# Kernel tuning notes

Hardware: AMD Instinct MI355X
Metric: run time of the kernel (lower is better)

The kernel has to match this reference:

```python
import jax, jax.numpy as jnp
import numpy as np

EMBEDDING_DIM = 64  # matches init_kwargs; temperature = sqrt(embedding_dim)


def setup_inputs() -> dict:
    key = jax.random.key(0)
    k1, k2, k3, k4 = jax.random.split(key, 4)
    B, S, D = 8, 2048, EMBEDDING_DIM
    return {
        "key": jax.random.normal(k1, (B, S, D), dtype=jnp.float32),
        "query": jax.random.normal(k2, (B, S, D), dtype=jnp.float32),
        "value": jax.random.normal(k3, (B, S, D), dtype=jnp.float32),
        "query_attention_mask": jax.random.randint(k4, (B, S), 0, 2, dtype=jnp.int32),
    }


def reference(key, query, value, query_attention_mask):
    # scores: [B, S, S]
    temperature = jnp.sqrt(jnp.asarray(EMBEDDING_DIM, dtype=query.dtype))
    scores = jnp.einsum("bqd,bkd->bqk", query, key) / temperature
    # masked_fill_ fills -inf WHERE mask is True (as in the torch source).
    # mask [B, S] -> broadcast over the query axis to [B, 1, S] -> [B, S, S].
    mask = query_attention_mask.astype(bool)[:, None, :]
    scores = jnp.where(mask, -jnp.inf, scores)
    attention_filter = jax.nn.softmax(scores, axis=-1)
    # dropout p=0.0 (deterministic reference) -> identity
    context = jnp.einsum("bqk,bkd->bqd", attention_filter, value)
    return (context, attention_filter)
```

## Files before the change

### kernel.cpp

```cpp
#include <hip/hip_runtime.h>
#include <hip/hip_bf16.h>
#include <math.h>


typedef short bf16x8 __attribute__((ext_vector_type(8)));
typedef short bf16x4 __attribute__((ext_vector_type(4)));
typedef float f32x4 __attribute__((ext_vector_type(4)));

#define BATCH 8
#define SDIM 2048
#define DDIM 64
#define KBLK 64
#define NBLK (SDIM / KBLK)
#define KSPLIT 4
#define BPW (NBLK / KSPLIT)
#define NROWS (BATCH * SDIM)
#define SCALE 0.125f
#define KSTR 66

__device__ __forceinline__ short f2bf(float f) {
    unsigned x = __float_as_uint(f);
    x = (x + 0x7fffu + ((x >> 16) & 1u)) >> 16;
    return (short)x;
}
__device__ __forceinline__ float fidx(const float4& v, int i) {
    return ((const float*)&v)[i];
}

__global__ __launch_bounds__(256, 4)
void attn_stats(const float* __restrict__ Kg, const float* __restrict__ Qg,
                const int* __restrict__ Mg, float* __restrict__ part)
{
    __shared__ short Klds[KBLK][KSTR];
    __shared__ int   Mlds[KBLK];

    const int wg = blockIdx.x;
    const int b = wg & 7;
    const int qt = (wg >> 3) & 31;
    const int sp = wg >> 8;
    const int tid = threadIdx.x;
    const int w = tid >> 6, lane = tid & 63, col = lane & 15, quad = lane >> 4;

    const float* Kb = Kg + (size_t)b * SDIM * DDIM;
    const float* Qb = Qg + (size_t)b * SDIM * DDIM;
    const int*   Mb = Mg + (size_t)b * SDIM;

    bf16x8 aq[2];
    {
        const float* qsrc = Qb + (size_t)(qt * 64 + w * 16 + col) * DDIM + quad * 8;
        #pragma unroll
        for (int c = 0; c < 2; ++c) {
            float4 f0 = *(const float4*)(qsrc + c * 32);
            float4 f1 = *(const float4*)(qsrc + c * 32 + 4);
            bf16x8 a;
            a[0]=f2bf(f0.x); a[1]=f2bf(f0.y); a[2]=f2bf(f0.z); a[3]=f2bf(f0.w);
            a[4]=f2bf(f1.x); a[5]=f2bf(f1.y); a[6]=f2bf(f1.z); a[7]=f2bf(f1.w);
            aq[c] = a;
        }
    }

    const int sk_key = tid >> 2;
    const int sk_d0  = (tid & 3) * 16;
    const int kb0 = sp * BPW * KBLK;

    float lsum[4];
    #pragma unroll
    for (int r = 0; r < 4; ++r) lsum[r] = 0.0f;

    float4 kreg[4];
    int mreg = 0;
    {
        const float* src = Kb + (size_t)(kb0 + sk_key) * DDIM + sk_d0;
        #pragma unroll
        for (int i = 0; i < 4; ++i) kreg[i] = *(const float4*)(src + i * 4);
        if (tid < KBLK) mreg = Mb[kb0 + tid];
    }

    for (int kb = 0; kb < BPW; ++kb) {
        __syncthreads();
        {
            bf16x8 p0, p1;
            p0[0]=f2bf(kreg[0].x); p0[1]=f2bf(kreg[0].y); p0[2]=f2bf(kreg[0].z); p0[3]=f2bf(kreg[0].w);
            p0[4]=f2bf(kreg[1].x); p0[5]=f2bf(kreg[1].y); p0[6]=f2bf(kreg[1].z); p0[7]=f2bf(kreg[1].w);
            p1[0]=f2bf(kreg[2].x); p1[1]=f2bf(kreg[2].y); p1[2]=f2bf(kreg[2].z); p1[3]=f2bf(kreg[2].w);
            p1[4]=f2bf(kreg[3].x); p1[5]=f2bf(kreg[3].y); p1[6]=f2bf(kreg[3].z); p1[7]=f2bf(kreg[3].w);
            *(bf16x8*)&Klds[sk_key][sk_d0]     = p0;
            *(bf16x8*)&Klds[sk_key][sk_d0 + 8] = p1;
            if (tid < KBLK) Mlds[tid] = mreg;
        }
        __syncthreads();
        if (kb + 1 < BPW) {
            const float* src = Kb + (size_t)(kb0 + (kb + 1) * KBLK + sk_key) * DDIM + sk_d0;
            #pragma unroll
            for (int i = 0; i < 4; ++i) kreg[i] = *(const float4*)(src + i * 4);
            if (tid < KBLK) mreg = Mb[kb0 + (kb + 1) * KBLK + tid];
        }

        #pragma unroll
        for (int t = 0; t < 4; ++t) {
            f32x4 acc = {0.f, 0.f, 0.f, 0.f};
            #pragma unroll
            for (int c = 0; c < 2; ++c) {
                bf16x8 bk = *(const bf16x8*)&Klds[t * 16 + col][c * 32 + quad * 8];
                acc = __builtin_amdgcn_mfma_f32_16x16x32_bf16(aq[c], bk, acc, 0, 0, 0);
            }
            const int mk = Mlds[t * 16 + col];
            #pragma unroll
            for (int r = 0; r < 4; ++r)
                lsum[r] += mk ? 0.0f : __expf(acc[r] * SCALE);
        }
    }

    #pragma unroll
    for (int r = 0; r < 4; ++r) {
        float s = lsum[r];
        s += __shfl_xor(s, 1);
        s += __shfl_xor(s, 2);
        s += __shfl_xor(s, 4);
        s += __shfl_xor(s, 8);
        lsum[r] = s;
    }
    if (col == 0) {
        #pragma unroll
        for (int r = 0; r < 4; ++r)
            part[(size_t)sp * NROWS + b * SDIM + qt * 64 + w * 16 + quad * 4 + r] = lsum[r];
    }
}

__global__ __launch_bounds__(256)
void attn_merge(const float* __restrict__ part, float* __restrict__ stats,
                float* __restrict__ Ctx)
{
    const int t = blockIdx.x * 256 + threadIdx.x;
    if (t < NROWS) {
        float l = part[t] + part[NROWS + t] + part[2 * NROWS + t] + part[3 * NROWS + t];
        stats[t] = 1.0f / l;
    }
    float4* C4 = (float4*)Ctx;
    const int n4 = BATCH * SDIM * DDIM / 4;
    const int nthr = gridDim.x * 256;
    for (int i = t; i < n4; i += nthr) C4[i] = make_float4(0.f, 0.f, 0.f, 0.f);
}

__global__ __launch_bounds__(256, 4)
void attn_emit(const float* __restrict__ Kg, const float* __restrict__ Vg,
               const float* __restrict__ Qg, const int* __restrict__ Mg,
               const float* __restrict__ stats, float* __restrict__ Ctx,
               float* __restrict__ Filt)
{
    __shared__ short Klds[KBLK][KSTR];
    __shared__ short VTlds[DDIM][KSTR];
    __shared__ short Plds[4][16][KSTR];
    __shared__ int   Mlds[KBLK];

    const int wg = blockIdx.x;
    const int b = wg & 7;
    const int qt = (wg >> 3) & 31;
    const int sp = wg >> 8;
    const int tid = threadIdx.x;
    const int w = tid >> 6, lane = tid & 63, col = lane & 15, quad = lane >> 4;

    const float* Kb = Kg + (size_t)b * SDIM * DDIM;
    const float* Qb = Qg + (size_t)b * SDIM * DDIM;
    const float* Vb = Vg + (size_t)b * SDIM * DDIM;
    const int*   Mb = Mg + (size_t)b * SDIM;
    float* Ctxb  = Ctx  + (size_t)b * SDIM * DDIM;
    float* Filtb = Filt + (size_t)b * SDIM * SDIM;

    bf16x8 aq[2];
    {
        const float* qsrc = Qb + (size_t)(qt * 64 + w * 16 + col) * DDIM + quad * 8;
        #pragma unroll
        for (int c = 0; c < 2; ++c) {
            float4 f0 = *(const float4*)(qsrc + c * 32);
            float4 f1 = *(const float4*)(qsrc + c * 32 + 4);
            bf16x8 a;
            a[0]=f2bf(f0.x); a[1]=f2bf(f0.y); a[2]=f2bf(f0.z); a[3]=f2bf(f0.w);
            a[4]=f2bf(f1.x); a[5]=f2bf(f1.y); a[6]=f2bf(f1.z); a[7]=f2bf(f1.w);
            aq[c] = a;
        }
    }

    float invl[4];
    #pragma unroll
    for (int r = 0; r < 4; ++r)
        invl[r] = stats[b * SDIM + qt * 64 + w * 16 + quad * 4 + r];

    const int sk_key = tid >> 2;
    const int sk_d0  = (tid & 3) * 16;
    const int sv_d0  = (tid & 15) * 4;
    const int sv_k0  = (tid >> 4) * 4;
    const int kb0 = sp * BPW * KBLK;

    f32x4 Oacc[4];
    #pragma unroll
    for (int dt = 0; dt < 4; ++dt) Oacc[dt] = (f32x4){0.f, 0.f, 0.f, 0.f};

    float4 kreg[4], vreg[4];
    int mreg = 0;
    {
        const float* srck = Kb + (size_t)(kb0 + sk_key) * DDIM + sk_d0;
        #pragma unroll
        for (int i = 0; i < 4; ++i) kreg[i] = *(const float4*)(srck + i * 4);
        const float* srcv = Vb + (size_t)(kb0 + sv_k0) * DDIM + sv_d0;
        #pragma unroll
        for (int i = 0; i < 4; ++i) vreg[i] = *(const float4*)(srcv + (size_t)i * DDIM);
        if (tid < KBLK) mreg = Mb[kb0 + tid];
    }

    for (int kb = 0; kb < BPW; ++kb) {
        const int kbase = kb0 + kb * KBLK;
        __syncthreads();
        {
            bf16x8 p0, p1;
            p0[0]=f2bf(kreg[0].x); p0[1]=f2bf(kreg[0].y); p0[2]=f2bf(kreg[0].z); p0[3]=f2bf(kreg[0].w);
            p0[4]=f2bf(kreg[1].x); p0[5]=f2bf(kreg[1].y); p0[6]=f2bf(kreg[1].z); p0[7]=f2bf(kreg[1].w);
            p1[0]=f2bf(kreg[2].x); p1[1]=f2bf(kreg[2].y); p1[2]=f2bf(kreg[2].z); p1[3]=f2bf(kreg[2].w);
            p1[4]=f2bf(kreg[3].x); p1[5]=f2bf(kreg[3].y); p1[6]=f2bf(kreg[3].z); p1[7]=f2bf(kreg[3].w);
            *(bf16x8*)&Klds[sk_key][sk_d0]     = p0;
            *(bf16x8*)&Klds[sk_key][sk_d0 + 8] = p1;
            #pragma unroll
            for (int dd = 0; dd < 4; ++dd) {
                bf16x4 pv;
                pv[0] = f2bf(fidx(vreg[0], dd));
                pv[1] = f2bf(fidx(vreg[1], dd));
                pv[2] = f2bf(fidx(vreg[2], dd));
                pv[3] = f2bf(fidx(vreg[3], dd));
                *(bf16x4*)&VTlds[sv_d0 + dd][sv_k0] = pv;
            }
            if (tid < KBLK) Mlds[tid] = mreg;
        }
        __syncthreads();
        if (kb + 1 < BPW) {
            const float* srck = Kb + (size_t)(kb0 + (kb + 1) * KBLK + sk_key) * DDIM + sk_d0;
            #pragma unroll
            for (int i = 0; i < 4; ++i) kreg[i] = *(const float4*)(srck + i * 4);
            const float* srcv = Vb + (size_t)(kb0 + (kb + 1) * KBLK + sv_k0) * DDIM + sv_d0;
            #pragma unroll
            for (int i = 0; i < 4; ++i) vreg[i] = *(const float4*)(srcv + (size_t)i * DDIM);
            if (tid < KBLK) mreg = Mb[kb0 + (kb + 1) * KBLK + tid];
        }

        #pragma unroll
        for (int t = 0; t < 4; ++t) {
            f32x4 acc = {0.f, 0.f, 0.f, 0.f};
            #pragma unroll
            for (int c = 0; c < 2; ++c) {
                bf16x8 bk = *(const bf16x8*)&Klds[t * 16 + col][c * 32 + quad * 8];
                acc = __builtin_amdgcn_mfma_f32_16x16x32_bf16(aq[c], bk, acc, 0, 0, 0);
            }
            const int mk = Mlds[t * 16 + col];
            #pragma unroll
            for (int r = 0; r < 4; ++r) {
                float p = mk ? 0.0f : __expf(acc[r] * SCALE) * invl[r];
                __builtin_nontemporal_store(
                    p, &Filtb[(size_t)(qt * 64 + w * 16 + quad * 4 + r) * SDIM + kbase + t * 16 + col]);
                Plds[w][quad * 4 + r][t * 16 + col] = f2bf(p);
            }
        }

        #pragma unroll
        for (int c = 0; c < 2; ++c) {
            bf16x8 ap = *(const bf16x8*)&Plds[w][col][c * 32 + quad * 8];
            #pragma unroll
            for (int dt = 0; dt < 4; ++dt) {
                bf16x8 bv = *(const bf16x8*)&VTlds[dt * 16 + col][c * 32 + quad * 8];
                Oacc[dt] = __builtin_amdgcn_mfma_f32_16x16x32_bf16(ap, bv, Oacc[dt], 0, 0, 0);
            }
        }
    }

    #pragma unroll
    for (int dt = 0; dt < 4; ++dt) {
        #pragma unroll
        for (int r = 0; r < 4; ++r) {
            unsafeAtomicAdd(&Ctxb[(size_t)(qt * 64 + w * 16 + quad * 4 + r) * DDIM + dt * 16 + col],
                            Oacc[dt][r]);
        }
    }
}

extern "C" void kernel_launch(void* const* d_in, const int* in_sizes, int n_in,
                              void* d_out, int out_size, void* d_ws, size_t ws_size,
                              hipStream_t stream) {
    const float* Kg = (const float*)d_in[0];
    const float* Qg = (const float*)d_in[1];
    const float* Vg = (const float*)d_in[2];
    const int*   Mg = (const int*)d_in[3];
    float* Ctx  = (float*)d_out;
    float* Filt = (float*)d_out + (size_t)BATCH * SDIM * DDIM;

    float* part  = (float*)d_ws;
    float* stats = part + (size_t)KSPLIT * NROWS;

    attn_stats<<<dim3(BATCH * NBLK * KSPLIT), dim3(256), 0, stream>>>(Kg, Qg, Mg, part);
    attn_merge<<<dim3(256), dim3(256), 0, stream>>>(part, stats, Ctx);
    attn_emit<<<dim3(BATCH * NBLK * KSPLIT), dim3(256), 0, stream>>>(Kg, Vg, Qg, Mg, stats, Ctx, Filt);
}
```

Measured before the change: 205.4 us.

## Precompute bf16 K and transposed V once in a prep kernel

Adds an attn_prep kernel that converts K to bf16 and V to a transposed bf16 layout in workspace, and zeroes the context output. The stats and emit kernels then load these pre-converted tiles directly into LDS instead of reloading fp32 data and converting per workgroup. This removes redundant conversion work and halves global read bytes for K/V across the 32 query-tile workgroups that reread them. It costs an extra launch and a workspace round trip. The LDS row stride also changes from 66 to 72.

```diff
diff --git a/kernel.cpp b/kernel.cpp
--- a/kernel.cpp
+++ b/kernel.cpp
@@ -16,7 +16,7 @@
 #define BPW (NBLK / KSPLIT)
 #define NROWS (BATCH * SDIM)
 #define SCALE 0.125f
-#define KSTR 66
+#define KSTR 72
 
 __device__ __forceinline__ short f2bf(float f) {
     unsigned x = __float_as_uint(f);
@@ -28,7 +28,71 @@
 }
 
 __global__ __launch_bounds__(256, 4)
-void attn_stats(const float* __restrict__ Kg, const float* __restrict__ Qg,
+void attn_prep(const float* __restrict__ Kg, const float* __restrict__ Vg,
+               short* __restrict__ Kbf, short* __restrict__ VTbf,
+               float* __restrict__ Ctx)
+{
+    __shared__ short VTlds[DDIM][KSTR];
+
+    const int wg = blockIdx.x;
+    const int b = wg & 7;
+    const int kbase = (wg >> 3) * KBLK;
+    const int tid = threadIdx.x;
+
+    const float* Kb = Kg + (size_t)b * SDIM * DDIM;
+    const float* Vb = Vg + (size_t)b * SDIM * DDIM;
+
+    {
+        const int key = tid >> 2, doff = (tid & 3) * 16;
+        const float* src = Kb + (size_t)(kbase + key) * DDIM + doff;
+        float4 f0 = *(const float4*)(src);
+        float4 f1 = *(const float4*)(src + 4);
+        float4 f2 = *(const float4*)(src + 8);
+        float4 f3 = *(const float4*)(src + 12);
+        bf16x8 p0, p1;
+        p0[0]=f2bf(f0.x); p0[1]=f2bf(f0.y); p0[2]=f2bf(f0.z); p0[3]=f2bf(f0.w);
+        p0[4]=f2bf(f1.x); p0[5]=f2bf(f1.y); p0[6]=f2bf(f1.z); p0[7]=f2bf(f1.w);
+        p1[0]=f2bf(f2.x); p1[1]=f2bf(f2.y); p1[2]=f2bf(f2.z); p1[3]=f2bf(f2.w);
+        p1[4]=f2bf(f3.x); p1[5]=f2bf(f3.y); p1[6]=f2bf(f3.z); p1[7]=f2bf(f3.w);
+        short* dst = Kbf + ((size_t)b * SDIM + kbase + key) * DDIM + doff;
+        *(bf16x8*)dst = p0;
+        *(bf16x8*)(dst + 8) = p1;
+    }
+
+    {
+        const int sv_d0 = (tid & 15) * 4, sv_k0 = (tid >> 4) * 4;
+        float4 vreg[4];
+        #pragma unroll
+        for (int i = 0; i < 4; ++i)
+            vreg[i] = *(const float4*)(Vb + (size_t)(kbase + sv_k0 + i) * DDIM + sv_d0);
+        #pragma unroll
+        for (int dd = 0; dd < 4; ++dd) {
+            bf16x4 pv;
+            pv[0] = f2bf(fidx(vreg[0], dd));
+            pv[1] = f2bf(fidx(vreg[1], dd));
+            pv[2] = f2bf(fidx(vreg[2], dd));
+            pv[3] = f2bf(fidx(vreg[3], dd));
+            *(bf16x4*)&VTlds[sv_d0 + dd][sv_k0] = pv;
+        }
+    }
+    __syncthreads();
+    {
+        const int d = tid >> 2, koff = (tid & 3) * 16;
+        bf16x8 a = *(const bf16x8*)&VTlds[d][koff];
+        bf16x8 c = *(const bf16x8*)&VTlds[d][koff + 8];
+        short* dst = VTbf + ((size_t)b * DDIM + d) * SDIM + kbase + koff;
+        *(bf16x8*)dst = a;
+        *(bf16x8*)(dst + 8) = c;
+    }
+
+    {
+        float4* dst = (float4*)Ctx + (size_t)wg * 1024;
+        for (int i = tid; i < 1024; i += 256) dst[i] = make_float4(0.f, 0.f, 0.f, 0.f);
+    }
+}
+
+__global__ __launch_bounds__(256, 4)
+void attn_stats(const short* __restrict__ Kbf, const float* __restrict__ Qg,
                 const int* __restrict__ Mg, float* __restrict__ part)
 {
     __shared__ short Klds[KBLK][KSTR];
@@ -41,7 +105,6 @@
     const int tid = threadIdx.x;
     const int w = tid >> 6, lane = tid & 63, col = lane & 15, quad = lane >> 4;
 
-    const float* Kb = Kg + (size_t)b * SDIM * DDIM;
     const float* Qb = Qg + (size_t)b * SDIM * DDIM;
     const int*   Mb = Mg + (size_t)b * SDIM;
 
@@ -59,40 +122,34 @@
         }
     }
 
-    const int sk_key = tid >> 2;
-    const int sk_d0  = (tid & 3) * 16;
+    const int skey = tid >> 2;
+    const int sdoff = (tid & 3) * 16;
     const int kb0 = sp * BPW * KBLK;
+    const short* Ksp = Kbf + ((size_t)b * SDIM + kb0) * DDIM;
 
     float lsum[4];
     #pragma unroll
     for (int r = 0; r < 4; ++r) lsum[r] = 0.0f;
 
-    float4 kreg[4];
+    bf16x8 ks0, ks1;
     int mreg = 0;
     {
-        const float* src = Kb + (size_t)(kb0 + sk_key) * DDIM + sk_d0;
-        #pragma unroll
-        for (int i = 0; i < 4; ++i) kreg[i] = *(const float4*)(src + i * 4);
+        const short* src = Ksp + (size_t)skey * DDIM + sdoff;
+        ks0 = *(const bf16x8*)src;
+        ks1 = *(const bf16x8*)(src + 8);
         if (tid < KBLK) mreg = Mb[kb0 + tid];
     }
 
     for (int kb = 0; kb < BPW; ++kb) {
         __syncthreads();
-        {
-            bf16x8 p0, p1;
-            p0[0]=f2bf(kreg[0].x); p0[1]=f2bf(kreg[0].y); p0[2]=f2bf(kreg[0].z); p0[3]=f2bf(kreg[0].w);
-            p0[4]=f2bf(kreg[1].x); p0[5]=f2bf(kreg[1].y); p0[6]=f2bf(kreg[1].z); p0[7]=f2bf(kreg[1].w);
-            p1[0]=f2bf(kreg[2].x); p1[1]=f2bf(kreg[2].y); p1[2]=f2bf(kreg[2].z); p1[3]=f2bf(kreg[2].w);
-            p1[4]=f2bf(kreg[3].x); p1[5]=f2bf(kreg[3].y); p1[6]=f2bf(kreg[3].z); p1[7]=f2bf(kreg[3].w);
-            *(bf16x8*)&Klds[sk_key][sk_d0]     = p0;
-            *(bf16x8*)&Klds[sk_key][sk_d0 + 8] = p1;
-            if (tid < KBLK) Mlds[tid] = mreg;
-        }
+        *(bf16x8*)&Klds[skey][sdoff]     = ks0;
+        *(bf16x8*)&Klds[skey][sdoff + 8] = ks1;
+        if (tid < KBLK) Mlds[tid] = mreg;
         __syncthreads();
         if (kb + 1 < BPW) {
-            const float* src = Kb + (size_t)(kb0 + (kb + 1) * KBLK + sk_key) * DDIM + sk_d0;
-            #pragma unroll
-            for (int i = 0; i < 4; ++i) kreg[i] = *(const float4*)(src + i * 4);
+            const short* src = Ksp + (size_t)((kb + 1) * KBLK + skey) * DDIM + sdoff;
+            ks0 = *(const bf16x8*)src;
+            ks1 = *(const bf16x8*)(src + 8);
             if (tid < KBLK) mreg = Mb[kb0 + (kb + 1) * KBLK + tid];
         }
 
@@ -128,22 +185,17 @@
 }
 
 __global__ __launch_bounds__(256)
-void attn_merge(const float* __restrict__ part, float* __restrict__ stats,
-                float* __restrict__ Ctx)
+void attn_merge(const float* __restrict__ part, float* __restrict__ stats)
 {
     const int t = blockIdx.x * 256 + threadIdx.x;
     if (t < NROWS) {
         float l = part[t] + part[NROWS + t] + part[2 * NROWS + t] + part[3 * NROWS + t];
         stats[t] = 1.0f / l;
     }
-    float4* C4 = (float4*)Ctx;
-    const int n4 = BATCH * SDIM * DDIM / 4;
-    const int nthr = gridDim.x * 256;
-    for (int i = t; i < n4; i += nthr) C4[i] = make_float4(0.f, 0.f, 0.f, 0.f);
 }
 
 __global__ __launch_bounds__(256, 4)
-void attn_emit(const float* __restrict__ Kg, const float* __restrict__ Vg,
+void attn_emit(const short* __restrict__ Kbf, const short* __restrict__ VTbf,
                const float* __restrict__ Qg, const int* __restrict__ Mg,
                const float* __restrict__ stats, float* __restrict__ Ctx,
                float* __restrict__ Filt)
@@ -160,9 +212,7 @@
     const int tid = threadIdx.x;
     const int w = tid >> 6, lane = tid & 63, col = lane & 15, quad = lane >> 4;
 
-    const float* Kb = Kg + (size_t)b * SDIM * DDIM;
     const float* Qb = Qg + (size_t)b * SDIM * DDIM;
-    const float* Vb = Vg + (size_t)b * SDIM * DDIM;
     const int*   Mb = Mg + (size_t)b * SDIM;
     float* Ctxb  = Ctx  + (size_t)b * SDIM * DDIM;
     float* Filtb = Filt + (size_t)b * SDIM * SDIM;
@@ -186,59 +236,46 @@
     for (int r = 0; r < 4; ++r)
         invl[r] = stats[b * SDIM + qt * 64 + w * 16 + quad * 4 + r];
 
-    const int sk_key = tid >> 2;
-    const int sk_d0  = (tid & 3) * 16;
-    const int sv_d0  = (tid & 15) * 4;
-    const int sv_k0  = (tid >> 4) * 4;
+    const int skey = tid >> 2;
+    const int sdoff = (tid & 3) * 16;
     const int kb0 = sp * BPW * KBLK;
+    const short* Ksp = Kbf + ((size_t)b * SDIM + kb0) * DDIM;
+    const short* VTb = VTbf + (size_t)b * DDIM * SDIM;
+    const int vd = tid >> 2, vkoff = (tid & 3) * 16;
 
     f32x4 Oacc[4];
     #pragma unroll
     for (int dt = 0; dt < 4; ++dt) Oacc[dt] = (f32x4){0.f, 0.f, 0.f, 0.f};
 
-    float4 kreg[4], vreg[4];
+    bf16x8 ks0, ks1, vt0, vt1;
     int mreg = 0;
     {
-        const float* srck = Kb + (size_t)(kb0 + sk_key) * DDIM + sk_d0;
-        #pragma unroll
-        for (int i = 0; i < 4; ++i) kreg[i] = *(const float4*)(srck + i * 4);
-        const float* srcv = Vb + (size_t)(kb0 + sv_k0) * DDIM + sv_d0;
-        #pragma unroll
-        for (int i = 0; i < 4; ++i) vreg[i] = *(const float4*)(srcv + (size_t)i * DDIM);
+        const short* srck = Ksp + (size_t)skey * DDIM + sdoff;
+        ks0 = *(const bf16x8*)srck;
+        ks1 = *(const bf16x8*)(srck + 8);
+        const short* srcv = VTb + (size_t)vd * SDIM + kb0 + vkoff;
+        vt0 = *(const bf16x8*)srcv;
+        vt1 = *(const bf16x8*)(srcv + 8);
         if (tid < KBLK) mreg = Mb[kb0 + tid];
     }
 
     for (int kb = 0; kb < BPW; ++kb) {
         const int kbase = kb0 + kb * KBLK;
         __syncthreads();
-        {
-            bf16x8 p0, p1;
-            p0[0]=f2bf(kreg[0].x); p0[1]=f2bf(kreg[0].y); p0[2]=f2bf(kreg[0].z); p0[3]=f2bf(kreg[0].w);
-            p0[4]=f2bf(kreg[1].x); p0[5]=f2bf(kreg[1].y); p0[6]=f2bf(kreg[1].z); p0[7]=f2bf(kreg[1].w);
-            p1[0]=f2bf(kreg[2].x); p1[1]=f2bf(kreg[2].y); p1[2]=f2bf(kreg[2].z); p1[3]=f2bf(kreg[2].w);
-            p1[4]=f2bf(kreg[3].x); p1[5]=f2bf(kreg[3].y); p1[6]=f2bf(kreg[3].z); p1[7]=f2bf(kreg[3].w);
-            *(bf16x8*)&Klds[sk_key][sk_d0]     = p0;
-            *(bf16x8*)&Klds[sk_key][sk_d0 + 8] = p1;
-            #pragma unroll
-            for (int dd = 0; dd < 4; ++dd) {
-                bf16x4 pv;
-                pv[0] = f2bf(fidx(vreg[0], dd));
-                pv[1] = f2bf(fidx(vreg[1], dd));
-                pv[2] = f2bf(fidx(vreg[2], dd));
-                pv[3] = f2bf(fidx(vreg[3], dd));
-                *(bf16x4*)&VTlds[sv_d0 + dd][sv_k0] = pv;
-            }
-            if (tid < KBLK) Mlds[tid] = mreg;
-        }
+        *(bf16x8*)&Klds[skey][sdoff]      = ks0;
+        *(bf16x8*)&Klds[skey][sdoff + 8]  = ks1;
+        *(bf16x8*)&VTlds[vd][vkoff]       = vt0;
+        *(bf16x8*)&VTlds[vd][vkoff + 8]   = vt1;
+        if (tid < KBLK) Mlds[tid] = mreg;
         __syncthreads();
         if (kb + 1 < BPW) {
-            const float* srck = Kb + (size_t)(kb0 + (kb + 1) * KBLK + sk_key) * DDIM + sk_d0;
-            #pragma unroll
-            for (int i = 0; i < 4; ++i) kreg[i] = *(const float4*)(srck + i * 4);
-            const float* srcv = Vb + (size_t)(kb0 + (kb + 1) * KBLK + sv_k0) * DDIM + sv_d0;
-            #pragma unroll
-            for (int i = 0; i < 4; ++i) vreg[i] = *(const float4*)(srcv + (size_t)i * DDIM);
-            if (tid < KBLK) mreg = Mb[kb0 + (kb + 1) * KBLK + tid];
+            const short* srck = Ksp + (size_t)((kb + 1) * KBLK + skey) * DDIM + sdoff;
+            ks0 = *(const bf16x8*)srck;
+            ks1 = *(const bf16x8*)(srck + 8);
+            const short* srcv = VTb + (size_t)vd * SDIM + (kbase + KBLK) + vkoff;
+            vt0 = *(const bf16x8*)srcv;
+            vt1 = *(const bf16x8*)(srcv + 8);
+            if (tid < KBLK) mreg = Mb[kbase + KBLK + tid];
         }
 
         #pragma unroll
@@ -290,10 +327,13 @@
     float* Ctx  = (float*)d_out;
     float* Filt = (float*)d_out + (size_t)BATCH * SDIM * DDIM;
 
-    float* part  = (float*)d_ws;
+    short* Kbf  = (short*)d_ws;
+    short* VTbf = Kbf + (size_t)BATCH * SDIM * DDIM;
+    float* part  = (float*)(VTbf + (size_t)BATCH * DDIM * SDIM);
     float* stats = part + (size_t)KSPLIT * NROWS;
 
-    attn_stats<<<dim3(BATCH * NBLK * KSPLIT), dim3(256), 0, stream>>>(Kg, Qg, Mg, part);
-    attn_merge<<<dim3(256), dim3(256), 0, stream>>>(part, stats, Ctx);
-    attn_emit<<<dim3(BATCH * NBLK * KSPLIT), dim3(256), 0, stream>>>(Kg, Vg, Qg, Mg, stats, Ctx, Filt);
-}
+    attn_prep<<<dim3(BATCH * NBLK), dim3(256), 0, stream>>>(Kg, Vg, Kbf, VTbf, Ctx);
+    attn_stats<<<dim3(BATCH * NBLK * KSPLIT), dim3(256), 0, stream>>>(Kbf, Qg, Mg, part);
+    attn_merge<<<dim3(NROWS / 256), dim3(256), 0, stream>>>(part, stats);
+    attn_emit<<<dim3(BATCH * NBLK * KSPLIT), dim3(256), 0, stream>>>(Kbf, VTbf, Qg, Mg, stats, Ctx, Filt);
+}
```

Result: faster. 187.9 us (-8.5%).
